# Optimization experiments

Measured on AMD Instinct MI355X. Metric: run time of the kernel, lower is better.

## Reference

```python
import jax, jax.numpy as jnp
import numpy as np
import math

B, S, H = 4, 2048, 1024
EMBED_DIM = 1024


def setup_inputs() -> dict:
    key = jax.random.key(0)
    ks = jax.random.split(key, 7)
    scale = 1.0 / math.sqrt(H)
    return {
        "xs": jax.random.normal(ks[0], (B, S, H), dtype=jnp.float32),
        "WQ_w": jax.random.normal(ks[1], (EMBED_DIM, H), dtype=jnp.float32) * scale,
        "WQ_b": jax.random.normal(ks[2], (EMBED_DIM,), dtype=jnp.float32) * scale,
        "WK_w": jax.random.normal(ks[3], (EMBED_DIM, H), dtype=jnp.float32) * scale,
        "WK_b": jax.random.normal(ks[4], (EMBED_DIM,), dtype=jnp.float32) * scale,
        "WV_w": jax.random.normal(ks[5], (EMBED_DIM, H), dtype=jnp.float32) * scale,
        "WV_b": jax.random.normal(ks[6], (EMBED_DIM,), dtype=jnp.float32) * scale,
    }


def reference(xs, WQ_w, WQ_b, WK_w, WK_b, WV_w, WV_b):
    # Linear projections (torch nn.Linear: x @ W.T + b)
    q = jnp.einsum('bsh,eh->bse', xs, WQ_w) + WQ_b  # [B,S,E]
    k = jnp.einsum('bsh,eh->bse', xs, WK_w) + WK_b
    v = jnp.einsum('bsh,eh->bse', xs, WV_w) + WV_b
    seq_len = xs.shape[1]
    inv_sqrt_e = 1.0 / math.sqrt(EMBED_DIM)
    qk = jnp.einsum('bqe,bke->bqk', q, k) * inv_sqrt_e  # [B,S,S]
    # causal mask: positions k > q get -inf (triu, diagonal=1)
    causal = jnp.tril(jnp.ones((seq_len, seq_len), dtype=bool))
    qk = jnp.where(causal[None, :, :], qk, -jnp.inf)
    attn = jax.nn.softmax(qk, axis=2)
    y = jnp.einsum('bqk,bke->bqe', attn, v)  # [B,S,E]
    return y
```

## Files before the change

### kernel.cpp

```cpp
#include <hip/hip_runtime.h>
#include <cstdint>
#include <cstddef>

typedef _Float16 f16;
typedef __attribute__((ext_vector_type(4))) _Float16 f16x4;
typedef __attribute__((ext_vector_type(8))) _Float16 f16x8;
typedef __attribute__((ext_vector_type(4))) float f32x4;

static constexpr int BB = 4;
static constexpr int SS = 2048;
static constexpr int EE = 1024;

static constexpr int BM = 128, BN = 128;

__device__ __forceinline__ void gload_lds16(const f16* g, f16* l) {
  __builtin_amdgcn_global_load_lds(
      (const __attribute__((address_space(1))) void*)g,
      (__attribute__((address_space(3))) void*)l, 16, 0, 0);
}

struct Frag {
  int lane, wave, wy, wx, l16, quad, quadx;
  __device__ Frag() {
    const int tid = threadIdx.x;
    lane = tid & 63; wave = tid >> 6;
    wy = wave >> 1; wx = wave & 1;
    l16 = lane & 15; quad = lane >> 4;
    quadx = quad ^ ((l16 >> 2) & 3);
  }
};

struct Stager {
  const f16* g[2];
  int l[2];
  __device__ void init(const f16* base, int ld, const Frag& fr) {
#pragma unroll
    for (int i = 0; i < 2; ++i) {
      const int c = fr.wave * 128 + i * 64 + fr.lane;
      const int row = c >> 2;
      const int kcs = (c & 3) ^ ((c >> 4) & 3);
      g[i] = base + (size_t)row * ld + kcs * 8;
      l[i] = c * 8;
    }
  }
  __device__ __forceinline__ void stage(int ko, f16* lds) const {
    gload_lds16(g[0] + ko, lds + l[0]);
    gload_lds16(g[1] + ko, lds + l[1]);
  }
};

__device__ __forceinline__ void mfma_round(
    const f16* __restrict__ Ash, const f16* __restrict__ Bsh,
    f32x4 acc[4][4], const Frag& fr)
{
  f16x8 af[4], bf[4];
#pragma unroll
  for (int mi = 0; mi < 4; ++mi)
    af[mi] = *(const f16x8*)(Ash + (fr.wy * 64 + mi * 16 + fr.l16) * 32 + fr.quadx * 8);
#pragma unroll
  for (int ni = 0; ni < 4; ++ni)
    bf[ni] = *(const f16x8*)(Bsh + (fr.wx * 64 + ni * 16 + fr.l16) * 32 + fr.quadx * 8);
#pragma unroll
  for (int mi = 0; mi < 4; ++mi)
#pragma unroll
    for (int ni = 0; ni < 4; ++ni)
      acc[mi][ni] = __builtin_amdgcn_mfma_f32_16x16x32_f16(af[mi], bf[ni], acc[mi][ni], 0, 0, 0);
}

__device__ __forceinline__ void gemm_core(
    const f16* __restrict__ A, const f16* __restrict__ Bt,
    int lda, int ldb, int kOuter,
    f16* __restrict__ Ash, f16* __restrict__ Bsh,
    f32x4 acc[4][4], const Frag& fr)
{
  Stager sa, sb;
  sa.init(A, lda, fr);
  sb.init(Bt, ldb, fr);
  for (int kt = 0; kt < kOuter; ++kt) {
    const int ko = kt * 64;
    sa.stage(ko, Ash);       sa.stage(ko + 32, Ash + 128 * 32);
    sb.stage(ko, Bsh);       sb.stage(ko + 32, Bsh + 128 * 32);
    __syncthreads();
    mfma_round(Ash, Bsh, acc, fr);
    mfma_round(Ash + 128 * 32, Bsh + 128 * 32, acc, fr);
    __syncthreads();
  }
}

__global__ __launch_bounds__(256) void cast_all_kernel(
    const float* __restrict__ xs,
    const float* __restrict__ w0, const float* __restrict__ w1, const float* __restrict__ w2,
    f16* __restrict__ Xh, f16* __restrict__ o0, f16* __restrict__ o1, f16* __restrict__ o2)
{
  const int i = blockIdx.x * 256 + threadIdx.x;
  const float* src; f16* dst; int idx;
  if (i < 2097152) {
    src = xs; dst = Xh; idx = i;
  } else {
    const int j = i - 2097152;
    const int w = j >> 18;
    idx = j & 262143;
    src = (w == 0) ? w0 : (w == 1) ? w1 : w2;
    dst = (w == 0) ? o0 : (w == 1) ? o1 : o2;
  }
  const float4 f = ((const float4*)src)[idx];
  f16x4 h;
  h.x = (f16)f.x; h.y = (f16)f.y; h.z = (f16)f.z; h.w = (f16)f.w;
  ((f16x4*)dst)[idx] = h;
}

__global__ __launch_bounds__(512, 1) void proj4_kernel(
    const f16* __restrict__ X,
    const f16* __restrict__ Wq, const f16* __restrict__ Wk, const f16* __restrict__ Wv,
    const float* __restrict__ bq, const float* __restrict__ bk, const float* __restrict__ bv,
    f16* __restrict__ Qh, f16* __restrict__ Kh, f16* __restrict__ Vt)
{
  __shared__ __align__(16) f16 smem[65536];
  const int tid = threadIdx.x;
  const int lane = tid & 63, wave = tid >> 6;
  const int wy = wave >> 2, wx = wave & 3;
  const int l16 = lane & 15, quad = lane >> 4;

  const int t = blockIdx.x;
  const int which = (t < 128) ? 0 : (t < 256) ? 1 : 2;
  const int u = t - which * 128;
  const int c8 = u & 7, g = u >> 3;
  const f16* Abase; const f16* Bbase;
  int mt, nt;
  if (which < 2) {
    mt = c8 + 8 * (g & 3);
    nt = g >> 2;
    Abase = X + (size_t)mt * 256 * EE;
    Bbase = ((which == 0) ? Wq : Wk) + (size_t)nt * 256 * EE;
  } else {
    nt = c8 + 8 * (g & 3);
    mt = g >> 2;
    Abase = Wv + (size_t)mt * 256 * EE;
    Bbase = X + (size_t)nt * 256 * EE;
  }

  const f16* gA[4]; const f16* gB[4]; int lc[4];
#pragma unroll
  for (int j = 0; j < 4; ++j) {
    const int slot = j * 512 + tid;
    const int r = slot >> 3, cg = (slot & 7) ^ (r & 7);
    gA[j] = Abase + (size_t)r * EE + cg * 8;
    gB[j] = Bbase + (size_t)r * EE + cg * 8;
    lc[j] = slot * 8;
  }

  auto stageTile = [&](int bi, int kt) {
    const int ko = kt * 64;
    f16* ab = smem + bi * 16384;
    f16* bb = smem + 32768 + bi * 16384;
#pragma unroll
    for (int j = 0; j < 4; ++j) gload_lds16(gA[j] + ko, ab + lc[j]);
#pragma unroll
    for (int j = 0; j < 4; ++j) gload_lds16(gB[j] + ko, bb + lc[j]);
  };

  int obA[2], obB[2];
#pragma unroll
  for (int ks = 0; ks < 2; ++ks) {
    const int rA = wy * 128 + l16;
    const int rB = wx * 64 + l16;
    obA[ks] = (rA * 8 + ((ks * 4 + quad) ^ (rA & 7))) * 8;
    obB[ks] = (rB * 8 + ((ks * 4 + quad) ^ (rB & 7))) * 8;
  }

  stageTile(0, 0);

  f32x4 acc[8][4] = {};

  constexpr int NT = 16;
  for (int kt = 0; kt < NT; ++kt) {
    const int cur = kt & 1, nxt = cur ^ 1;
    __builtin_amdgcn_s_barrier();
    if (kt + 1 < NT) {
      stageTile(nxt, kt + 1);
      asm volatile("s_waitcnt vmcnt(8)" ::: "memory");
    } else {
      asm volatile("s_waitcnt vmcnt(0)" ::: "memory");
    }
    __builtin_amdgcn_s_barrier();

    const f16* Ac = smem + cur * 16384;
    const f16* Bc = smem + 32768 + cur * 16384;
#pragma unroll
    for (int ks = 0; ks < 2; ++ks) {
      f16x8 a[8], b[4];
#pragma unroll
      for (int mi = 0; mi < 8; ++mi) a[mi] = *(const f16x8*)(Ac + obA[ks] + mi * 1024);
#pragma unroll
      for (int ni = 0; ni < 4; ++ni) b[ni] = *(const f16x8*)(Bc + obB[ks] + ni * 1024);
      __builtin_amdgcn_s_setprio(1);
#pragma unroll
      for (int mi = 0; mi < 8; ++mi)
#pragma unroll
        for (int ni = 0; ni < 4; ++ni)
          acc[mi][ni] = __builtin_amdgcn_mfma_f32_16x16x32_f16(a[mi], b[ni], acc[mi][ni], 0, 0, 0);
      __builtin_amdgcn_s_setprio(0);
    }
  }

  const int r0 = mt * 256 + wy * 128;
  const int c0 = nt * 256 + wx * 64;
  if (which < 2) {
    const float* bias = (which == 0) ? bq : bk;
    f16* out = (which == 0) ? Qh : Kh;
#pragma unroll
    for (int ni = 0; ni < 4; ++ni) {
      const int c = c0 + ni * 16 + l16;
      const float bz = bias[c];
#pragma unroll
      for (int mi = 0; mi < 8; ++mi) {
        const int r = r0 + mi * 16 + quad * 4;
#pragma unroll
        for (int i = 0; i < 4; ++i)
          out[(size_t)(r + i) * EE + c] = (f16)(acc[mi][ni][i] + bz);
      }
    }
  } else {
#pragma unroll
    for (int ni = 0; ni < 4; ++ni) {
      const int cg = c0 + ni * 16 + l16;
      const int b = cg >> 11, sc = cg & 2047;
      f16* out = Vt + (size_t)b * EE * SS;
#pragma unroll
      for (int mi = 0; mi < 8; ++mi) {
        const int r = r0 + mi * 16 + quad * 4;
#pragma unroll
        for (int i = 0; i < 4; ++i)
          out[(size_t)(r + i) * SS + sc] = (f16)(acc[mi][ni][i] + bv[r + i]);
      }
    }
  }
}

__global__ __launch_bounds__(256) void scores_kernel(
    const f16* __restrict__ Q, const f16* __restrict__ Kh, f16* __restrict__ Sc)
{
  __shared__ __align__(16) f16 Ash[2][BM * 32];
  __shared__ __align__(16) f16 Bsh[2][BN * 32];
  const int t = blockIdx.x, b = blockIdx.z;
  int qt = 0;
  while ((qt + 1) * (qt + 2) / 2 <= t) ++qt;
  const int kt = t - qt * (qt + 1) / 2;
  const f16* A  = Q  + (size_t)b * SS * EE + (size_t)qt * BM * EE;
  const f16* Bp = Kh + (size_t)b * SS * EE + (size_t)kt * BN * EE;
  f16* out = Sc + (size_t)b * SS * SS;
  Frag fr;
  f32x4 acc[4][4] = {};
  gemm_core(A, Bp, EE, EE, EE / 64, Ash[0], Bsh[0], acc, fr);
  const float scale = 0.03125f;
#pragma unroll
  for (int ni = 0; ni < 4; ++ni) {
    const int c = kt * BN + fr.wx * 64 + ni * 16 + fr.l16;
#pragma unroll
    for (int mi = 0; mi < 4; ++mi) {
      const int r = qt * BM + fr.wy * 64 + mi * 16 + fr.quad * 4;
#pragma unroll
      for (int i = 0; i < 4; ++i)
        out[(size_t)(r + i) * SS + c] = (f16)(acc[mi][ni][i] * scale);
    }
  }
}

__global__ __launch_bounds__(256) void softmax_kernel(f16* __restrict__ Sc)
{
  const int q = blockIdx.x, b = blockIdx.y;
  f16* row = Sc + (size_t)b * SS * SS + (size_t)q * SS;
  const int n = q + 1;
  const int kend = ((q >> 7) + 1) << 7;
  const int tid = threadIdx.x;
  const int i0 = tid * 8;

  float v[8];
  if (i0 + 8 <= n) {
    const f16x8 h = *(const f16x8*)(row + i0);
#pragma unroll
    for (int j = 0; j < 8; ++j) v[j] = (float)h[j];
  } else {
#pragma unroll
    for (int j = 0; j < 8; ++j) {
      const int idx = i0 + j;
      v[j] = (idx < n) ? (float)row[idx] : -1e30f;
    }
  }

  float m = v[0];
#pragma unroll
  for (int j = 1; j < 8; ++j) m = fmaxf(m, v[j]);
  __shared__ float red[4];
#pragma unroll
  for (int off = 32; off > 0; off >>= 1) m = fmaxf(m, __shfl_down(m, off));
  if ((tid & 63) == 0) red[tid >> 6] = m;
  __syncthreads();
  m = fmaxf(fmaxf(red[0], red[1]), fmaxf(red[2], red[3]));

  float sum = 0.f;
#pragma unroll
  for (int j = 0; j < 8; ++j) {
    v[j] = (i0 + j < n) ? __expf(v[j] - m) : 0.f;
    sum += v[j];
  }
#pragma unroll
  for (int off = 32; off > 0; off >>= 1) sum += __shfl_down(sum, off);
  __syncthreads();
  if ((tid & 63) == 0) red[tid >> 6] = sum;
  __syncthreads();
  sum = red[0] + red[1] + red[2] + red[3];
  const float inv = 1.f / sum;

  if (i0 < kend) {
    f16x8 h;
#pragma unroll
    for (int j = 0; j < 8; ++j) h[j] = (f16)(v[j] * inv);
    *(f16x8*)(row + i0) = h;
  }
}

__global__ __launch_bounds__(256) void pv_kernel(
    const f16* __restrict__ P, const f16* __restrict__ Vt, float* __restrict__ Y)
{
  __shared__ __align__(16) f16 Ash[2][BM * 32];
  __shared__ __align__(16) f16 Bsh[2][BN * 32];
  const int t = blockIdx.x;
  const int u = t & 255;
  const int qh = u & 7, et = (u >> 3) & 7, b = u >> 6;
  const int qt = (t < 256) ? (15 - qh) : qh;
  const f16* A  = P  + (size_t)b * SS * SS + (size_t)qt * BM * SS;
  const f16* Bp = Vt + (size_t)b * EE * SS + (size_t)et * BN * SS;
  float* out = Y + (size_t)b * SS * EE;
  Frag fr;
  f32x4 acc[4][4] = {};
  gemm_core(A, Bp, SS, SS, (qt + 1) * 2, Ash[0], Bsh[0], acc, fr);
#pragma unroll
  for (int ni = 0; ni < 4; ++ni) {
    const int c = et * BN + fr.wx * 64 + ni * 16 + fr.l16;
#pragma unroll
    for (int mi = 0; mi < 4; ++mi) {
      const int r = qt * BM + fr.wy * 64 + mi * 16 + fr.quad * 4;
#pragma unroll
      for (int i = 0; i < 4; ++i)
        out[(size_t)(r + i) * EE + c] = acc[mi][ni][i];
    }
  }
}

extern "C" void kernel_launch(void* const* d_in, const int* in_sizes, int n_in,
                              void* d_out, int out_size, void* d_ws, size_t ws_size,
                              hipStream_t stream)
{
  const float* xs  = (const float*)d_in[0];
  const float* WQw = (const float*)d_in[1];
  const float* WQb = (const float*)d_in[2];
  const float* WKw = (const float*)d_in[3];
  const float* WKb = (const float*)d_in[4];
  const float* WVw = (const float*)d_in[5];
  const float* WVb = (const float*)d_in[6];

  const size_t ME = (size_t)BB * SS * EE;
  const size_t WE = (size_t)EE * EE;

  f16* Xh = (f16*)d_ws;
  f16* Wq = Xh + ME;
  f16* Wk = Wq + WE;
  f16* Wv = Wk + WE;
  f16* Qh = Wv + WE;
  f16* Kh = Qh + ME;
  f16* Vt = Kh + ME;
  f16* Sc = Vt + ME;

  cast_all_kernel<<<dim3(11264), 256, 0, stream>>>(
      xs, WQw, WKw, WVw, Xh, Wq, Wk, Wv);

  proj4_kernel<<<dim3(384), 512, 0, stream>>>(
      Xh, Wq, Wk, Wv, WQb, WKb, WVb, Qh, Kh, Vt);

  const int nTri = (SS / BM) * (SS / BM + 1) / 2;
  scores_kernel<<<dim3(nTri, 1, BB), 256, 0, stream>>>(Qh, Kh, Sc);

  softmax_kernel<<<dim3(SS, BB), 256, 0, stream>>>(Sc);

  pv_kernel<<<dim3(512), 256, 0, stream>>>(Sc, Vt, (float*)d_out);
}
```

Before: 261.4 us.

## Restructure projection GEMM main loop into half-tile staged 8-wave ping-pong pipeline

```diff
diff --git a/kernel.cpp b/kernel.cpp
--- a/kernel.cpp
+++ b/kernel.cpp
@@ -109,7 +109,7 @@
   ((f16x4*)dst)[idx] = h;
 }
 
-__global__ __launch_bounds__(512, 1) void proj4_kernel(
+__global__ __launch_bounds__(512, 1) void proj5_kernel(
     const f16* __restrict__ X,
     const f16* __restrict__ Wq, const f16* __restrict__ Wk, const f16* __restrict__ Wv,
     const float* __restrict__ bq, const float* __restrict__ bk, const float* __restrict__ bv,
@@ -139,69 +139,115 @@
     Bbase = X + (size_t)nt * 256 * EE;
   }
 
-  const f16* gA[4]; const f16* gB[4]; int lc[4];
-#pragma unroll
-  for (int j = 0; j < 4; ++j) {
-    const int slot = j * 512 + tid;
-    const int r = slot >> 3, cg = (slot & 7) ^ (r & 7);
-    gA[j] = Abase + (size_t)r * EE + cg * 8;
-    gB[j] = Bbase + (size_t)r * EE + cg * 8;
-    lc[j] = slot * 8;
-  }
-
-  auto stageTile = [&](int bi, int kt) {
-    const int ko = kt * 64;
-    f16* ab = smem + bi * 16384;
-    f16* bb = smem + 32768 + bi * 16384;
-#pragma unroll
-    for (int j = 0; j < 4; ++j) gload_lds16(gA[j] + ko, ab + lc[j]);
-#pragma unroll
-    for (int j = 0; j < 4; ++j) gload_lds16(gB[j] + ko, bb + lc[j]);
+  const f16* gA[2][2]; const f16* gB[2][2]; int lso[2];
+#pragma unroll
+  for (int j = 0; j < 2; ++j) {
+    const int s = j * 512 + tid;
+    const int r = s >> 3, cg = (s & 7) ^ (r & 7);
+    lso[j] = s * 8;
+#pragma unroll
+    for (int h = 0; h < 2; ++h) {
+      gA[h][j] = Abase + (size_t)(h * 128 + r) * EE + cg * 8;
+      gB[h][j] = Bbase + (size_t)(h * 128 + r) * EE + cg * 8;
+    }
+  }
+
+  auto stA = [&](int h, int x) {
+    if (x < 16) {
+      const int ko = x * 64;
+      f16* dst = smem + ((x & 1) * 2 + h) * 8192;
+      gload_lds16(gA[h][0] + ko, dst + lso[0]);
+      gload_lds16(gA[h][1] + ko, dst + lso[1]);
+    }
   };
+  auto stB = [&](int h, int x) {
+    if (x < 16) {
+      const int ko = x * 64;
+      f16* dst = smem + 32768 + ((x & 1) * 2 + h) * 8192;
+      gload_lds16(gB[h][0] + ko, dst + lso[0]);
+      gload_lds16(gB[h][1] + ko, dst + lso[1]);
+    }
+  };
 
   int obA[2], obB[2];
 #pragma unroll
   for (int ks = 0; ks < 2; ++ks) {
-    const int rA = wy * 128 + l16;
-    const int rB = wx * 64 + l16;
-    obA[ks] = (rA * 8 + ((ks * 4 + quad) ^ (rA & 7))) * 8;
+    const int rB = (wx & 1) * 64 + l16;
+    obA[ks] = (l16 * 8 + ((ks * 4 + quad) ^ (l16 & 7))) * 8;
     obB[ks] = (rB * 8 + ((ks * 4 + quad) ^ (rB & 7))) * 8;
   }
 
-  stageTile(0, 0);
+#define PBAR() asm volatile("s_barrier" ::: "memory")
+#define LGKM0() do { asm volatile("s_waitcnt lgkmcnt(0)" ::: "memory"); \
+                     __builtin_amdgcn_sched_barrier(0); } while (0)
+#define QUAD(MH, NH, AF, BF) do { \
+  __builtin_amdgcn_s_setprio(1); \
+  _Pragma("unroll") for (int m = 0; m < 4; ++m) \
+  _Pragma("unroll") for (int n = 0; n < 2; ++n) \
+  _Pragma("unroll") for (int ks = 0; ks < 2; ++ks) \
+    acc[(MH)*4+m][(NH)*2+n] = __builtin_amdgcn_mfma_f32_16x16x32_f16( \
+        AF[m][ks], BF[n][ks], acc[(MH)*4+m][(NH)*2+n], 0, 0, 0); \
+  __builtin_amdgcn_s_setprio(0); } while (0)
+
+  stB(0, 0); stB(1, 0); stA(0, 0); stA(1, 0);
+  stB(0, 1); stB(1, 1);
+  asm volatile("s_waitcnt vmcnt(4)" ::: "memory");
+  __builtin_amdgcn_s_barrier();
 
   f32x4 acc[8][4] = {};
 
-  constexpr int NT = 16;
-  for (int kt = 0; kt < NT; ++kt) {
-    const int cur = kt & 1, nxt = cur ^ 1;
-    __builtin_amdgcn_s_barrier();
-    if (kt + 1 < NT) {
-      stageTile(nxt, kt + 1);
-      asm volatile("s_waitcnt vmcnt(8)" ::: "memory");
-    } else {
-      asm volatile("s_waitcnt vmcnt(0)" ::: "memory");
-    }
-    __builtin_amdgcn_s_barrier();
-
-    const f16* Ac = smem + cur * 16384;
-    const f16* Bc = smem + 32768 + cur * 16384;
-#pragma unroll
-    for (int ks = 0; ks < 2; ++ks) {
-      f16x8 a[8], b[4];
-#pragma unroll
-      for (int mi = 0; mi < 8; ++mi) a[mi] = *(const f16x8*)(Ac + obA[ks] + mi * 1024);
-#pragma unroll
-      for (int ni = 0; ni < 4; ++ni) b[ni] = *(const f16x8*)(Bc + obB[ks] + ni * 1024);
-      __builtin_amdgcn_s_setprio(1);
-#pragma unroll
-      for (int mi = 0; mi < 8; ++mi)
-#pragma unroll
-        for (int ni = 0; ni < 4; ++ni)
-          acc[mi][ni] = __builtin_amdgcn_mfma_f32_16x16x32_f16(a[mi], b[ni], acc[mi][ni], 0, 0, 0);
-      __builtin_amdgcn_s_setprio(0);
-    }
-  }
+  for (int i = 0; i < 8; ++i) {
+    const bool last = (i == 7);
+#pragma unroll
+    for (int h2 = 0; h2 < 2; ++h2) {
+      const int Tx = h2 ? 2 * i + 2 : 2 * i + 1;
+      const int Ty = h2 ? 2 * i + 3 : 2 * i + 2;
+      const f16* Ard = smem + (h2 * 2 + wy) * 8192;
+      const f16* Brd = smem + 32768 + (h2 * 2 + (wx >> 1)) * 8192;
+      f16x8 a0[4][2], a1[4][2], b0[2][2], b1[2][2];
+
+#pragma unroll
+      for (int m = 0; m < 4; ++m)
+#pragma unroll
+        for (int ks = 0; ks < 2; ++ks) a0[m][ks] = *(const f16x8*)(Ard + obA[ks] + m * 1024);
+#pragma unroll
+      for (int n = 0; n < 2; ++n)
+#pragma unroll
+        for (int ks = 0; ks < 2; ++ks) b0[n][ks] = *(const f16x8*)(Brd + obB[ks] + n * 1024);
+      stA(0, Tx);
+      PBAR(); LGKM0();
+      QUAD(0, 0, a0, b0);
+      PBAR();
+
+#pragma unroll
+      for (int n = 0; n < 2; ++n)
+#pragma unroll
+        for (int ks = 0; ks < 2; ++ks) b1[n][ks] = *(const f16x8*)(Brd + obB[ks] + (n + 2) * 1024);
+      stA(1, Tx);
+      PBAR(); LGKM0();
+      QUAD(0, 1, a0, b1);
+      PBAR();
+
+#pragma unroll
+      for (int m = 0; m < 4; ++m)
+#pragma unroll
+        for (int ks = 0; ks < 2; ++ks) a1[m][ks] = *(const f16x8*)(Ard + obA[ks] + (m + 4) * 1024);
+      stB(0, Ty);
+      PBAR(); LGKM0();
+      QUAD(1, 1, a1, b1);
+      PBAR();
+
+      stB(1, Ty);
+      if (last && h2 == 0)      asm volatile("s_waitcnt vmcnt(0)" ::: "memory");
+      else if (!(last && h2 == 1)) asm volatile("s_waitcnt vmcnt(4)" ::: "memory");
+      PBAR();
+      QUAD(1, 0, a1, b0);
+      PBAR();
+    }
+  }
+#undef PBAR
+#undef LGKM0
+#undef QUAD
 
   const int r0 = mt * 256 + wy * 128;
   const int c0 = nt * 256 + wx * 64;
@@ -375,7 +421,7 @@
   cast_all_kernel<<<dim3(11264), 256, 0, stream>>>(
       xs, WQw, WKw, WVw, Xh, Wq, Wk, Wv);
 
-  proj4_kernel<<<dim3(384), 512, 0, stream>>>(
+  proj5_kernel<<<dim3(384), 512, 0, stream>>>(
       Xh, Wq, Wk, Wv, WQb, WKb, WVb, Qh, Kh, Vt);
 
   const int nTri = (SS / BM) * (SS / BM + 1) / 2;
```

New measurement: 258.7 us. About the same (-1.0%).
